# Kernel tuning notes

Measured on AMD Instinct MI355X. Metric: run time of the kernel, lower is better.

## Reference

```python
import jax, jax.numpy as jnp
import numpy as np

DIM = 1024
NUM_HEADS = 16
HEAD_DIM = DIM // NUM_HEADS


def setup_inputs() -> dict:
    key = jax.random.key(0)
    k_x, k_qkv, k_proj, k_b = jax.random.split(key, 4)
    B, N, P, C = 4, 96, 64, DIM
    x = jax.random.normal(k_x, (B, N, P, C), dtype=jnp.float32)
    # nn.Linear(dim, 3*dim, bias=False): store as (in, out) for x @ W
    s = 1.0 / np.sqrt(C)
    W_qkv = jax.random.uniform(k_qkv, (C, 3 * C), minval=-s, maxval=s, dtype=jnp.float32)
    W_proj = jax.random.uniform(k_proj, (C, C), minval=-s, maxval=s, dtype=jnp.float32)
    b_proj = jax.random.uniform(k_b, (C,), minval=-s, maxval=s, dtype=jnp.float32)
    return {"x": x, "W_qkv": W_qkv, "W_proj": W_proj, "b_proj": b_proj}


def reference(x, W_qkv, W_proj, b_proj):
    B, N, P, C = x.shape
    H, hd = NUM_HEADS, C // NUM_HEADS
    # qkv projection: (B,N,P,3C) -> (B,N,P,3,H,hd)
    qkv = (x @ W_qkv).reshape(B, N, P, 3, H, hd)
    # q,k: mean-pool over patches P -> (B,H,N,hd)
    q = qkv[..., 0, :, :].mean(axis=2).transpose(0, 2, 1, 3)
    k = qkv[..., 1, :, :].mean(axis=2).transpose(0, 2, 1, 3)
    # v keeps all patches: (B,N,P,H,hd) -> (B,H,N,hd,P) -> (B,H,N,hd*P)
    v = qkv[..., 2, :, :].transpose(0, 3, 1, 4, 2).reshape(B, H, N, hd * P)
    # SDPA with default scale 1/sqrt(q_last_dim) = 1/sqrt(hd)
    scores = jnp.einsum('bhnd,bhmd->bhnm', q, k) * (hd ** -0.5)
    attn = jax.nn.softmax(scores, axis=-1)
    out = jnp.einsum('bhnm,bhme->bhne', attn, v)  # e = hd*P
    # unflatten back to (B,N,P,C)
    out = out.reshape(B, H, N, hd, P).transpose(0, 2, 4, 1, 3).reshape(B, N, P, C)
    return out @ W_proj + b_proj
```

## Files before the change

kernel.cpp:

```cpp
#include <hip/hip_runtime.h>
#include <cstdint>
#include <cstddef>

#define PPP  64
#define CC   1024

typedef __attribute__((ext_vector_type(8))) short short8;
typedef __attribute__((ext_vector_type(4))) float floatx4;
typedef __attribute__((ext_vector_type(4))) unsigned short ushort4v;

__device__ inline float bf2f(unsigned short u) {
  union { unsigned int i; float f; } v; v.i = ((unsigned int)u) << 16; return v.f;
}
__device__ inline unsigned short f2bf(float f) {
  union { float f; unsigned int i; } v; v.f = f;
  unsigned int x = v.i;
  unsigned int r = (x + 0x7fffu + ((x >> 16) & 1u)) >> 16;
  return (unsigned short)r;
}

#define GLD16(gp, lp)                                                          \
  __builtin_amdgcn_global_load_lds(                                            \
      (const __attribute__((address_space(1))) void*)(gp),                     \
      (__attribute__((address_space(3))) void*)(lp), 16, 0, 0)

__global__ __launch_bounds__(256) void conv_mean(
    const float* __restrict__ x, unsigned short* __restrict__ xbf,
    unsigned short* __restrict__ xm) {
  int bn = blockIdx.x;
  int c4 = threadIdx.x * 4;
  const float* xp = x + (size_t)bn * (PPP * CC) + c4;
  unsigned short* xo = xbf + (size_t)bn * (PPP * CC) + c4;
  float4 s = {0.f, 0.f, 0.f, 0.f};
#pragma unroll 8
  for (int p = 0; p < PPP; ++p) {
    float4 v = *(const float4*)&xp[(size_t)p * CC];
    s.x += v.x; s.y += v.y; s.z += v.z; s.w += v.w;
    ushort4v pk;
    pk.x = f2bf(v.x); pk.y = f2bf(v.y); pk.z = f2bf(v.z); pk.w = f2bf(v.w);
    *(ushort4v*)&xo[(size_t)p * CC] = pk;
  }
  ushort4v pm;
  pm.x = f2bf(s.x * (1.0f / PPP)); pm.y = f2bf(s.y * (1.0f / PPP));
  pm.z = f2bf(s.z * (1.0f / PPP)); pm.w = f2bf(s.w * (1.0f / PPP));
  *(ushort4v*)&xm[(size_t)bn * CC + c4] = pm;
}

__global__ __launch_bounds__(256) void transpose_f32_bf16(
    const float* __restrict__ src, unsigned short* __restrict__ dst,
    int R, int Cc, int src_stride) {
  __shared__ unsigned short tile[32][33];
  int tc = blockIdx.x * 32, tr = blockIdx.y * 32;
  int tx = threadIdx.x & 31, ty = threadIdx.x >> 5;
  for (int yy = ty; yy < 32; yy += 8)
    tile[yy][tx] = f2bf(src[(size_t)(tr + yy) * src_stride + tc + tx]);
  __syncthreads();
  for (int yy = ty; yy < 32; yy += 8)
    dst[(size_t)(tc + yy) * R + tr + tx] = tile[tx][yy];
}

template <bool F32OUT, bool SWIZ>
__global__ __launch_bounds__(256) void gemm_bt(
    const unsigned short* __restrict__ A, const unsigned short* __restrict__ BT,
    void* __restrict__ Cout, const float* __restrict__ bias,
    int M, int N, int K, int nbx) {
  __shared__ unsigned short As[128 * 32];
  __shared__ unsigned short Bs[128 * 32];

  int bx, by;
  {
    int bid = blockIdx.x;
    if (SWIZ) {
      bx = (bid >> 3) & 7;
      by = (bid & 7) * (gridDim.x >> 6) + (bid >> 6);
    } else {
      bx = bid % nbx;
      by = bid / nbx;
    }
  }
  const int rowBase = by * 128;
  const int colBase = bx * 128;
  const int t = threadIdx.x;
  const int wave = t >> 6, lane = t & 63;
  const int qr = wave >> 1, qc = wave & 1;
  const int m16 = lane & 15, quad = lane >> 4;

  floatx4 acc[4][4];
#pragma unroll
  for (int i = 0; i < 4; ++i)
#pragma unroll
    for (int j = 0; j < 4; ++j) {
      acc[i][j][0] = 0.f; acc[i][j][1] = 0.f; acc[i][j][2] = 0.f; acc[i][j][3] = 0.f;
    }

  for (int k0 = 0; k0 < K; k0 += 32) {
    __syncthreads();
#pragma unroll
    for (int u = 0; u < 2; ++u) {
      int ch = (u * 4 + wave) * 64 + lane;
      int row = ch >> 2, c8 = (ch & 3) << 3;
      GLD16(&A [(size_t)(rowBase + row) * K + k0 + c8], &As[ch * 8]);
      GLD16(&BT[(size_t)(colBase + row) * K + k0 + c8], &Bs[ch * 8]);
    }
    __syncthreads();

    short8 af[4], bfr[4];
#pragma unroll
    for (int i = 0; i < 4; ++i)
      af[i] = *(const short8*)&As[(qr * 64 + i * 16 + m16) * 32 + quad * 8];
#pragma unroll
    for (int j = 0; j < 4; ++j)
      bfr[j] = *(const short8*)&Bs[(qc * 64 + j * 16 + m16) * 32 + quad * 8];
#pragma unroll
    for (int i = 0; i < 4; ++i)
#pragma unroll
      for (int j = 0; j < 4; ++j)
        acc[i][j] = __builtin_amdgcn_mfma_f32_16x16x32_bf16(af[i], bfr[j], acc[i][j], 0, 0, 0);
  }

  float bv[4];
#pragma unroll
  for (int j = 0; j < 4; ++j)
    bv[j] = bias ? bias[colBase + qc * 64 + j * 16 + m16] : 0.f;

#pragma unroll
  for (int i = 0; i < 4; ++i) {
    int row0 = rowBase + qr * 64 + i * 16 + quad * 4;
#pragma unroll
    for (int j = 0; j < 4; ++j) {
      int col = colBase + qc * 64 + j * 16 + m16;
#pragma unroll
      for (int r = 0; r < 4; ++r) {
        float f = acc[i][j][r] + bv[j];
        if (F32OUT)
          ((float*)Cout)[(size_t)(row0 + r) * N + col] = f;
        else
          ((unsigned short*)Cout)[(size_t)(row0 + r) * N + col] = f2bf(f);
      }
    }
  }
}

template <bool F32OUT>
__global__ __launch_bounds__(512, 2) void gemm_bt256(
    const unsigned short* __restrict__ A, const unsigned short* __restrict__ BT,
    void* __restrict__ Cout, const float* __restrict__ bias,
    int M, int N, int K) {
  __shared__ __attribute__((aligned(16))) unsigned short As[2][256 * 64];
  __shared__ __attribute__((aligned(16))) unsigned short Bs[2][256 * 64];

  const int nbx = N >> 8;
  int tid = (blockIdx.x & 7) * (gridDim.x >> 3) + (blockIdx.x >> 3);
  const int bx = tid % nbx, by = tid / nbx;
  const int rowBase = by * 256, colBase = bx * 256;

  const int t = threadIdx.x;
  const int wave = t >> 6, lane = t & 63;
  const int wr = wave >> 2, wc = wave & 3;
  const int m16 = lane & 15, quad = lane >> 4;
  const int sw7 = m16 & 7;

  const unsigned short* srcA[4];
  int offA[4];
#pragma unroll
  for (int u = 0; u < 4; ++u) {
    int c = u * 512 + t;
    int row = c >> 3, pch = c & 7;
    int l = pch ^ (row & 7);
    srcA[u] = A + (size_t)(rowBase + row) * K + l * 8;
    offA[u] = c * 8;
  }
  const unsigned short* srcB[2][2];
  int offB[2][2];
#pragma unroll
  for (int g = 0; g < 2; ++g)
#pragma unroll
    for (int u = 0; u < 2; ++u) {
      int i = u * 512 + t;
      int col = g * 32 + ((i >> 8) << 6) + ((i >> 3) & 31);
      int kcp = i & 7;
      int l = kcp ^ (col & 7);
      srcB[g][u] = BT + (size_t)(colBase + col) * K + l * 8;
      offB[g][u] = col * 64 + kcp * 8;
    }

  floatx4 acc[8][4];
#pragma unroll
  for (int i = 0; i < 8; ++i)
#pragma unroll
    for (int j = 0; j < 4; ++j) {
      acc[i][j][0] = 0.f; acc[i][j][1] = 0.f; acc[i][j][2] = 0.f; acc[i][j][3] = 0.f;
    }

  short8 ar[4][2];
  short8 br[2][2][2];

#define RD_A(buf, qa)                                                          \
  _Pragma("unroll") for (int i_ = 0; i_ < 4; ++i_)                             \
  _Pragma("unroll") for (int kh_ = 0; kh_ < 2; ++kh_)                          \
    ar[i_][kh_] = *(const short8*)&As[buf][                                    \
        (wr * 128 + (qa) * 64 + i_ * 16 + m16) * 64 +                          \
        (((kh_ * 4 + quad) ^ sw7) * 8)];
#define RD_B(buf, qb)                                                          \
  _Pragma("unroll") for (int j_ = 0; j_ < 2; ++j_)                             \
  _Pragma("unroll") for (int kh_ = 0; kh_ < 2; ++kh_)                          \
    br[qb][j_][kh_] = *(const short8*)&Bs[buf][                                \
        (wc * 64 + (qb) * 32 + j_ * 16 + m16) * 64 +                           \
        (((kh_ * 4 + quad) ^ sw7) * 8)];
#define MFMA_PH(qa, qb)                                                        \
  __builtin_amdgcn_sched_barrier(0);                                           \
  __builtin_amdgcn_s_setprio(1);                                               \
  _Pragma("unroll") for (int kh_ = 0; kh_ < 2; ++kh_)                          \
  _Pragma("unroll") for (int i_ = 0; i_ < 4; ++i_)                             \
  _Pragma("unroll") for (int j_ = 0; j_ < 2; ++j_)                             \
    acc[(qa) * 4 + i_][(qb) * 2 + j_] =                                        \
        __builtin_amdgcn_mfma_f32_16x16x32_bf16(                               \
            ar[i_][kh_], br[qb][j_][kh_], acc[(qa) * 4 + i_][(qb) * 2 + j_],   \
            0, 0, 0);                                                          \
  __builtin_amdgcn_s_setprio(0);                                               \
  __builtin_amdgcn_sched_barrier(0);
#define WAITV(n) asm volatile("s_waitcnt vmcnt(" #n ")" ::: "memory")
#define BAR() asm volatile("s_barrier" ::: "memory")

  GLD16(srcA[0], &As[0][offA[0]]);
  GLD16(srcA[2], &As[0][offA[2]]);
  GLD16(srcB[0][0], &Bs[0][offB[0][0]]);
  GLD16(srcB[0][1], &Bs[0][offB[0][1]]);
  GLD16(srcB[1][0], &Bs[0][offB[1][0]]);
  GLD16(srcB[1][1], &Bs[0][offB[1][1]]);
  GLD16(srcA[1], &As[0][offA[1]]);
  GLD16(srcA[3], &As[0][offA[3]]);

  const int NT = K >> 6;
  int cur = 0;
#pragma unroll 1
  for (int kt = 0; kt < NT - 1; ++kt, cur ^= 1) {
    const int nxt = cur ^ 1;
    const int ko = (kt + 1) << 6;
    WAITV(4); BAR();
    RD_A(cur, 0); RD_B(cur, 0);
    GLD16(srcA[0] + ko, &As[nxt][offA[0]]);
    GLD16(srcA[2] + ko, &As[nxt][offA[2]]);
    MFMA_PH(0, 0);
    WAITV(4); BAR();
    RD_B(cur, 1);
    GLD16(srcB[0][0] + ko, &Bs[nxt][offB[0][0]]);
    GLD16(srcB[0][1] + ko, &Bs[nxt][offB[0][1]]);
    MFMA_PH(0, 1);
    WAITV(4); BAR();
    RD_A(cur, 1);
    GLD16(srcB[1][0] + ko, &Bs[nxt][offB[1][0]]);
    GLD16(srcB[1][1] + ko, &Bs[nxt][offB[1][1]]);
    MFMA_PH(1, 0);
    GLD16(srcA[1] + ko, &As[nxt][offA[1]]);
    GLD16(srcA[3] + ko, &As[nxt][offA[3]]);
    MFMA_PH(1, 1);
  }
  WAITV(4); BAR();
  RD_A(cur, 0); RD_B(cur, 0);
  MFMA_PH(0, 0);
  WAITV(2); BAR();
  RD_B(cur, 1);
  MFMA_PH(0, 1);
  WAITV(0); BAR();
  RD_A(cur, 1);
  MFMA_PH(1, 0);
  MFMA_PH(1, 1);

#undef RD_A
#undef RD_B
#undef MFMA_PH
#undef WAITV
#undef BAR

  float bv[4];
#pragma unroll
  for (int jg = 0; jg < 4; ++jg)
    bv[jg] = bias ? bias[colBase + wc * 64 + jg * 16 + m16] : 0.f;

#pragma unroll
  for (int ig = 0; ig < 8; ++ig) {
    int row0 = rowBase + wr * 128 + ig * 16 + quad * 4;
#pragma unroll
    for (int jg = 0; jg < 4; ++jg) {
      int col = colBase + wc * 64 + jg * 16 + m16;
#pragma unroll
      for (int r = 0; r < 4; ++r) {
        float f = acc[ig][jg][r] + bv[jg];
        if (F32OUT)
          ((float*)Cout)[(size_t)(row0 + r) * N + col] = f;
        else
          ((unsigned short*)Cout)[(size_t)(row0 + r) * N + col] = f2bf(f);
      }
    }
  }
}

__global__ __launch_bounds__(128) void softmax_k(
    const float* __restrict__ qk, unsigned short* __restrict__ attn) {
  int bh = blockIdx.x;
  int b = bh >> 4, h = bh & 15;
  __shared__ float ks[96][64];
  __shared__ float sc[96][96];
  int t = threadIdx.x;
  for (int idx = t; idx < 96 * 64; idx += 128) {
    int n = idx >> 6, d = idx & 63;
    ks[n][d] = qk[(size_t)(b * 96 + n) * 2048 + 1024 + h * 64 + d];
  }
  __syncthreads();
  if (t < 96) {
    float qreg[64];
    const float* qrow = qk + (size_t)(b * 96 + t) * 2048 + h * 64;
#pragma unroll
    for (int d = 0; d < 64; ++d) qreg[d] = qrow[d];

    float mx = -1e30f;
    for (int m = 0; m < 96; ++m) {
      float s0 = 0.f, s1 = 0.f, s2 = 0.f, s3 = 0.f;
#pragma unroll
      for (int d = 0; d < 64; d += 4) {
        s0 += qreg[d + 0] * ks[m][d + 0];
        s1 += qreg[d + 1] * ks[m][d + 1];
        s2 += qreg[d + 2] * ks[m][d + 2];
        s3 += qreg[d + 3] * ks[m][d + 3];
      }
      float s = ((s0 + s1) + (s2 + s3)) * 0.125f;
      sc[m][t] = s;
      mx = fmaxf(mx, s);
    }
    float sum = 0.f;
    for (int m = 0; m < 96; ++m) {
      float e = __expf(sc[m][t] - mx);
      sc[m][t] = e;
      sum += e;
    }
    float inv = 1.0f / sum;
    size_t base = (size_t)(bh * 96 + t) * 96;
    for (int m = 0; m < 96; ++m) attn[base + m] = f2bf(sc[m][t] * inv);
  }
}

__global__ __launch_bounds__(256) void attn_apply_mfma(
    const unsigned short* __restrict__ attn, const unsigned short* __restrict__ V,
    unsigned short* __restrict__ out2) {
  const int bid = blockIdx.x;
  const int bh = bid >> 5, ct = bid & 31;
  const int b = bh >> 4;
  const int t = threadIdx.x;
  const int wave = t >> 6, lane = t & 63;
  const int m16 = lane & 15, quad = lane >> 4;

  const unsigned short* An = attn + (size_t)bh * 96 * 96;
  const int vb = b * 96 * 64 * CC;

  floatx4 acc[6][2];
#pragma unroll
  for (int i = 0; i < 6; ++i)
#pragma unroll
    for (int j = 0; j < 2; ++j) {
      acc[i][j][0] = 0.f; acc[i][j][1] = 0.f; acc[i][j][2] = 0.f; acc[i][j][3] = 0.f;
    }

  int p_[2], base_[2];
#pragma unroll
  for (int jj = 0; jj < 2; ++jj) {
    int colL = wave * 32 + jj * 16;
    int p = ct * 2 + (colL >> 6);
    int d = (colL & 63) + m16;
    p_[jj] = p;
    base_[jj] = vb + p * CC + ((bh & 15) * 64) + d;
  }

#pragma unroll
  for (int k0 = 0; k0 < 96; k0 += 32) {
    short8 af[6];
#pragma unroll
    for (int i = 0; i < 6; ++i)
      af[i] = *(const short8*)&An[(i * 16 + m16) * 96 + k0 + quad * 8];
#pragma unroll
    for (int jj = 0; jj < 2; ++jj) {
      short8 bfr;
#pragma unroll
      for (int j = 0; j < 8; ++j)
        bfr[j] = (short)V[(size_t)base_[jj] + (size_t)(k0 + quad * 8 + j) * (64 * CC)];
#pragma unroll
      for (int i = 0; i < 6; ++i)
        acc[i][jj] = __builtin_amdgcn_mfma_f32_16x16x32_bf16(af[i], bfr, acc[i][jj], 0, 0, 0);
    }
  }

#pragma unroll
  for (int jj = 0; jj < 2; ++jj) {
    int colL = wave * 32 + jj * 16;
    int d = (colL & 63) + m16;
    size_t obase = (size_t)(b * 96) * 64 * CC + (size_t)p_[jj] * CC + (bh & 15) * 64 + d;
#pragma unroll
    for (int i = 0; i < 6; ++i) {
#pragma unroll
      for (int r = 0; r < 4; ++r) {
        int n = i * 16 + quad * 4 + r;
        out2[obase + (size_t)n * (64 * CC)] = f2bf(acc[i][jj][r]);
      }
    }
  }
}

extern "C" void kernel_launch(void* const* d_in, const int* in_sizes, int n_in,
                              void* d_out, int out_size, void* d_ws, size_t ws_size,
                              hipStream_t stream) {
  const float* x      = (const float*)d_in[0];
  const float* W_qkv  = (const float*)d_in[1];
  const float* W_proj = (const float*)d_in[2];
  const float* b_proj = (const float*)d_in[3];
  float* out = (float*)d_out;

  char* w = (char*)d_ws;
  unsigned short* WqkvT = (unsigned short*)(w);
  unsigned short* WpT   = (unsigned short*)(w + 6291456);
  unsigned short* xm    = (unsigned short*)(w + 8388608);
  float*          qkbuf = (float*)(w + 9175040);
  unsigned short* attn  = (unsigned short*)(w + 12320768);
  unsigned short* out2w = (unsigned short*)(w + 13500416);
  unsigned short* xbf   = (unsigned short*)d_out;
  unsigned short* Vbuf  = (unsigned short*)((char*)d_out + 50331648);

  const bool fullws = ws_size >= (size_t)13500416 + 50331648;

  conv_mean<<<dim3(384), 256, 0, stream>>>(x, xbf, xm);

  transpose_f32_bf16<<<dim3(96, 32), 256, 0, stream>>>(W_qkv, WqkvT, 1024, 3072, 3072);
  transpose_f32_bf16<<<dim3(32, 32), 256, 0, stream>>>(W_proj, WpT, 1024, 1024, 1024);

  gemm_bt<true, false><<<dim3(48), 256, 0, stream>>>(
      xm, WqkvT, qkbuf, nullptr, 384, 2048, 1024, 16);

  softmax_k<<<dim3(64), 128, 0, stream>>>(qkbuf, attn);

  gemm_bt256<false><<<dim3(384), 512, 0, stream>>>(
      xbf, WqkvT + (size_t)2048 * 1024, Vbuf, nullptr, 24576, 1024, 1024);

  if (fullws) {
    attn_apply_mfma<<<dim3(2048), 256, 0, stream>>>(attn, Vbuf, out2w);
    gemm_bt256<true><<<dim3(384), 512, 0, stream>>>(
        out2w, WpT, out, b_proj, 24576, 1024, 1024);
  } else {
    for (int b = 0; b < 4; ++b) {
      attn_apply_mfma<<<dim3(512), 256, 0, stream>>>(
          attn + (size_t)b * 16 * 96 * 96,
          Vbuf + (size_t)b * 6144 * 1024,
          out2w);
      gemm_bt256<true><<<dim3(96), 512, 0, stream>>>(
          out2w, WpT, out + (size_t)b * 6144 * 1024, b_proj, 6144, 1024, 1024);
    }
  }
}
```

Before: 386.5 us.

## Triple-buffer B tiles and cut GEMM main loop to one barrier

```diff
diff --git a/kernel.cpp b/kernel.cpp
--- a/kernel.cpp
+++ b/kernel.cpp
@@ -147,7 +147,7 @@
     void* __restrict__ Cout, const float* __restrict__ bias,
     int M, int N, int K) {
   __shared__ __attribute__((aligned(16))) unsigned short As[2][256 * 64];
-  __shared__ __attribute__((aligned(16))) unsigned short Bs[2][256 * 64];
+  __shared__ __attribute__((aligned(16))) unsigned short Bs[3][256 * 64];
 
   const int nbx = N >> 8;
   int tid = (blockIdx.x & 7) * (gridDim.x >> 3) + (blockIdx.x >> 3);
@@ -208,7 +208,6 @@
         (wc * 64 + (qb) * 32 + j_ * 16 + m16) * 64 +                           \
         (((kh_ * 4 + quad) ^ sw7) * 8)];
 #define MFMA_PH(qa, qb)                                                        \
-  __builtin_amdgcn_sched_barrier(0);                                           \
   __builtin_amdgcn_s_setprio(1);                                               \
   _Pragma("unroll") for (int kh_ = 0; kh_ < 2; ++kh_)                          \
   _Pragma("unroll") for (int i_ = 0; i_ < 4; ++i_)                             \
@@ -217,53 +216,63 @@
         __builtin_amdgcn_mfma_f32_16x16x32_bf16(                               \
             ar[i_][kh_], br[qb][j_][kh_], acc[(qa) * 4 + i_][(qb) * 2 + j_],   \
             0, 0, 0);                                                          \
-  __builtin_amdgcn_s_setprio(0);                                               \
-  __builtin_amdgcn_sched_barrier(0);
+  __builtin_amdgcn_s_setprio(0);
 #define WAITV(n) asm volatile("s_waitcnt vmcnt(" #n ")" ::: "memory")
-#define BAR() asm volatile("s_barrier" ::: "memory")
-
+#define BARR() asm volatile("s_barrier" ::: "memory")
+#define FEN() asm volatile("" ::: "memory")
+
+  GLD16(srcB[0][0], &Bs[0][offB[0][0]]);
+  GLD16(srcB[0][1], &Bs[0][offB[0][1]]); FEN();
+  GLD16(srcB[1][0], &Bs[0][offB[1][0]]);
+  GLD16(srcB[1][1], &Bs[0][offB[1][1]]); FEN();
   GLD16(srcA[0], &As[0][offA[0]]);
-  GLD16(srcA[2], &As[0][offA[2]]);
-  GLD16(srcB[0][0], &Bs[0][offB[0][0]]);
-  GLD16(srcB[0][1], &Bs[0][offB[0][1]]);
-  GLD16(srcB[1][0], &Bs[0][offB[1][0]]);
-  GLD16(srcB[1][1], &Bs[0][offB[1][1]]);
+  GLD16(srcA[2], &As[0][offA[2]]); FEN();
   GLD16(srcA[1], &As[0][offA[1]]);
-  GLD16(srcA[3], &As[0][offA[3]]);
+  GLD16(srcA[3], &As[0][offA[3]]); FEN();
+  GLD16(srcB[0][0] + 64, &Bs[1][offB[0][0]]);
+  GLD16(srcB[0][1] + 64, &Bs[1][offB[0][1]]); FEN();
+  GLD16(srcB[1][0] + 64, &Bs[1][offB[1][0]]);
+  GLD16(srcB[1][1] + 64, &Bs[1][offB[1][1]]); FEN();
 
   const int NT = K >> 6;
-  int cur = 0;
+  int acur = 0, bcur = 0;
 #pragma unroll 1
-  for (int kt = 0; kt < NT - 1; ++kt, cur ^= 1) {
-    const int nxt = cur ^ 1;
-    const int ko = (kt + 1) << 6;
-    WAITV(4); BAR();
-    RD_A(cur, 0); RD_B(cur, 0);
-    GLD16(srcA[0] + ko, &As[nxt][offA[0]]);
-    GLD16(srcA[2] + ko, &As[nxt][offA[2]]);
+  for (int kt = 0; kt < NT - 1; ++kt) {
+    const int anxt = acur ^ 1;
+    const int bnx2 = (bcur >= 1) ? bcur - 1 : 2;
+    const int koA = (kt + 1) << 6;
+    const int koB = (kt + 2) << 6;
+    const bool doB = (kt + 2) < NT;
+    WAITV(4); BARR();
+    RD_A(acur, 0);
+    RD_B(bcur, 0);
+    RD_B(bcur, 1);
+    GLD16(srcA[0] + koA, &As[anxt][offA[0]]);
+    GLD16(srcA[2] + koA, &As[anxt][offA[2]]); FEN();
     MFMA_PH(0, 0);
-    WAITV(4); BAR();
-    RD_B(cur, 1);
-    GLD16(srcB[0][0] + ko, &Bs[nxt][offB[0][0]]);
-    GLD16(srcB[0][1] + ko, &Bs[nxt][offB[0][1]]);
+    GLD16(srcA[1] + koA, &As[anxt][offA[1]]);
+    GLD16(srcA[3] + koA, &As[anxt][offA[3]]); FEN();
     MFMA_PH(0, 1);
-    WAITV(4); BAR();
-    RD_A(cur, 1);
-    GLD16(srcB[1][0] + ko, &Bs[nxt][offB[1][0]]);
-    GLD16(srcB[1][1] + ko, &Bs[nxt][offB[1][1]]);
+    RD_A(acur, 1);
+    if (doB) {
+      GLD16(srcB[0][0] + koB, &Bs[bnx2][offB[0][0]]);
+      GLD16(srcB[0][1] + koB, &Bs[bnx2][offB[0][1]]);
+    }
+    FEN();
     MFMA_PH(1, 0);
-    GLD16(srcA[1] + ko, &As[nxt][offA[1]]);
-    GLD16(srcA[3] + ko, &As[nxt][offA[3]]);
+    if (doB) {
+      GLD16(srcB[1][0] + koB, &Bs[bnx2][offB[1][0]]);
+      GLD16(srcB[1][1] + koB, &Bs[bnx2][offB[1][1]]);
+    }
+    FEN();
     MFMA_PH(1, 1);
-  }
-  WAITV(4); BAR();
-  RD_A(cur, 0); RD_B(cur, 0);
+    acur = anxt; bcur = (bcur == 2) ? 0 : bcur + 1;
+  }
+  WAITV(0); BARR();
+  RD_A(acur, 0); RD_B(bcur, 0); RD_B(bcur, 1);
   MFMA_PH(0, 0);
-  WAITV(2); BAR();
-  RD_B(cur, 1);
   MFMA_PH(0, 1);
-  WAITV(0); BAR();
-  RD_A(cur, 1);
+  RD_A(acur, 1);
   MFMA_PH(1, 0);
   MFMA_PH(1, 1);
 
@@ -271,7 +280,8 @@
 #undef RD_B
 #undef MFMA_PH
 #undef WAITV
-#undef BAR
+#undef BARR
+#undef FEN
 
   float bv[4];
 #pragma unroll
```

Measured after the change: 389.5 us. Within noise of the previous version (+0.8%).
